# Optimization experiments

Measured on AMD Instinct MI355X. Metric: run time of the kernel, lower is better.

Reference implementation:

```python
import jax, jax.numpy as jnp
import numpy as np

B = 8192          # batch
DIM = 2048        # feature dim
FANOUT = 10       # balanced 10-ary tree, depth 3 -> 1000 leaves
N_NODES = 1 + 10 + 100  # inner nodes with classifiers = 111
NUM_CLASSES = 1000


def setup_inputs() -> dict:
    key = jax.random.key(0)
    k1, k2, k3, k4 = jax.random.split(key, 4)
    x = jax.random.normal(k1, (B, DIM), dtype=jnp.float32)
    labels = jax.random.randint(k2, (B,), 0, NUM_CLASSES, dtype=jnp.int64 if jax.config.jax_enable_x64 else jnp.int32)
    # Stacked per-node Linear(dim, num_child+1): column 0 is the extra slot
    # included in the softmax but never routed to (children use cols 1..FANOUT).
    W = jax.random.normal(k3, (N_NODES, DIM, FANOUT + 1), dtype=jnp.float32) * (1.0 / np.sqrt(DIM))
    b = jax.random.normal(k4, (N_NODES, FANOUT + 1), dtype=jnp.float32) * 0.01
    return {"x": x, "labels": labels, "W": W, "b": b}


def reference(x, labels, W, b):
    # All 111 tiny per-node Linear+softmax classifiers fused into one batched GEMM.
    logits = jnp.einsum('bd,ndk->bnk', x, W) + b          # [B, 111, 11]
    probs = jax.nn.softmax(logits, axis=-1)               # softmax over num_child+1 (incl. dummy col 0)
    # Hierarchical path probabilities (root.path_prob = 1.0):
    # level-1 nodes are children of root (node 0), via softmax columns 1..10.
    p1 = probs[:, 0, 1:]                                   # [B, 10]
    # level-2 nodes: children of nodes 1..10
    p2 = (p1[:, :, None] * probs[:, 1:11, 1:]).reshape(x.shape[0], 100)    # [B, 100]
    # leaves: children of nodes 11..110 -> 1000 classes (out[:, 1:] slice already applied)
    out = (p2[:, :, None] * probs[:, 11:111, 1:]).reshape(x.shape[0], NUM_CLASSES)  # [B, 1000]
    penalty = jnp.float32(0.0)
    return (out, penalty)
```

## Files before the change

kernel.cpp:

```cpp
#include <hip/hip_runtime.h>
#include <hip/hip_bf16.h>
#include <hip/hip_fp16.h>

typedef _Float16 f16;
typedef __attribute__((ext_vector_type(8))) _Float16 f16x8;
typedef __attribute__((ext_vector_type(4))) float f32x4;

#define DIM     2048
#define BROWS   8192
#define NCOLS   1221
#define NPAD    1280
#define NNODES  111
#define BM      128
#define BN      128
#define BK      64
#define NKT     (DIM / BK)
#define MT      (BROWS / BM)
#define NT      (NPAD / BN)

__global__ __launch_bounds__(256) void prep_x(const float* __restrict__ X,
                                              f16* __restrict__ Xf) {
    __shared__ float T[128 * 68];
    int blk = blockIdx.x;
    int mt = blk >> 5, kt = blk & 31;
    int t = threadIdx.x;
    int row = t >> 1, half = t & 1;
    const float* src = X + (size_t)(mt * 128 + row) * DIM + kt * 64 + half * 32;
    float* dst = T + row * 68 + half * 32;
    #pragma unroll
    for (int i = 0; i < 8; ++i) ((f32x4*)dst)[i] = ((const f32x4*)src)[i];
    __syncthreads();
    int w = t >> 6, l = t & 63, r = l & 15, q = l >> 4;
    f16* out = Xf + (size_t)blk * 8192;
    #pragma unroll
    for (int p = 0; p < 4; ++p) {
        int gk = p * 4 + w;
        int kk = gk >> 3, g = gk & 7;
        const float* s = T + (g * 16 + r) * 68 + kk * 32 + q * 8;
        f32x4 a = *(const f32x4*)s;
        f32x4 b = *(const f32x4*)(s + 4);
        f16x8 h;
        h[0] = (f16)a[0]; h[1] = (f16)a[1]; h[2] = (f16)a[2]; h[3] = (f16)a[3];
        h[4] = (f16)b[0]; h[5] = (f16)b[1]; h[6] = (f16)b[2]; h[7] = (f16)b[3];
        *(f16x8*)(out + (size_t)(p * 256 + t) * 8) = h;
    }
}

__global__ void prep_b(const float* __restrict__ W, f16* __restrict__ Bf) {
    int idx = blockIdx.x * 256 + threadIdx.x;
    int c = idx & 1023, img = idx >> 10;
    int nt = img >> 5, kt = img & 31;
    int kk = c >> 9, g = (c >> 6) & 7, l = c & 63, r = l & 15, q = l >> 4;
    int col = nt * 128 + g * 16 + r;
    int d0  = kt * 64 + kk * 32 + q * 8;
    f16x8 v;
    if (col < NCOLS) {
        int n = col / 11, k = col - n * 11;
        const float* src = W + ((size_t)n * DIM + d0) * 11 + k;
        #pragma unroll
        for (int e = 0; e < 8; ++e) v[e] = (f16)src[(size_t)e * 11];
    } else {
        #pragma unroll
        for (int e = 0; e < 8; ++e) v[e] = (f16)0.f;
    }
    *(f16x8*)(Bf + (size_t)idx * 8) = v;
}

__global__ __launch_bounds__(512) void gemm_f16(const f16* __restrict__ Xf,
                                                const f16* __restrict__ Bf,
                                                f16* __restrict__ Lh) {
    __shared__ __align__(16) f16 As[2][8192];
    __shared__ __align__(16) f16 Bs[2][8192];

    int bid = blockIdx.x;
    int swz = (bid & 7) * 80 + (bid >> 3);
    int mt = swz / 10, nt = swz - mt * 10;

    int t = threadIdx.x, w = t >> 6, l = t & 63, r = l & 15, q = l >> 4;
    int wm = w >> 2, wn = w & 3;

    const f16* abase = Xf + (size_t)(mt * 32) * 8192 + (size_t)t * 8;
    const f16* bbase = Bf + (size_t)(nt * 32) * 8192 + (size_t)t * 8;

    f32x4 acc[4][2];
    #pragma unroll
    for (int i = 0; i < 4; ++i)
        #pragma unroll
        for (int j = 0; j < 2; ++j) acc[i][j] = (f32x4)0.f;

#define STAGE(KT, C)                                                             \
    {                                                                            \
        const f16* asrc = abase + (size_t)(KT) * 8192;                           \
        const f16* bsrc = bbase + (size_t)(KT) * 8192;                           \
        _Pragma("unroll")                                                        \
        for (int p = 0; p < 2; ++p) {                                            \
            __builtin_amdgcn_global_load_lds(                                    \
                (const __attribute__((address_space(1))) void*)(asrc + p * 4096),\
                (__attribute__((address_space(3))) void*)(&As[C][p * 4096 + w * 512]), 16, 0, 0); \
            __builtin_amdgcn_global_load_lds(                                    \
                (const __attribute__((address_space(1))) void*)(bsrc + p * 4096),\
                (__attribute__((address_space(3))) void*)(&Bs[C][p * 4096 + w * 512]), 16, 0, 0); \
        }                                                                        \
    }

#define COMPUTE(C)                                                               \
    {                                                                            \
        _Pragma("unroll")                                                        \
        for (int kk = 0; kk < 2; ++kk) {                                         \
            f16x8 af[4], bfr[2];                                                 \
            _Pragma("unroll")                                                    \
            for (int m = 0; m < 4; ++m)                                          \
                af[m] = *(const f16x8*)(&As[C][((kk * 8 + wm * 4 + m) * 64 + l) * 8]); \
            _Pragma("unroll")                                                    \
            for (int n = 0; n < 2; ++n)                                          \
                bfr[n] = *(const f16x8*)(&Bs[C][((kk * 8 + wn * 2 + n) * 64 + l) * 8]); \
            _Pragma("unroll")                                                    \
            for (int m = 0; m < 4; ++m)                                          \
                _Pragma("unroll")                                                \
                for (int n = 0; n < 2; ++n)                                      \
                    acc[m][n] = __builtin_amdgcn_mfma_f32_16x16x32_f16(af[m], bfr[n], acc[m][n], 0, 0, 0); \
        }                                                                        \
    }

#define STEP(KTCUR, CC, CN)                                                      \
    {                                                                            \
        STAGE(KTCUR + 1, CN)                                                     \
        asm volatile("s_waitcnt vmcnt(4)" ::: "memory");                         \
        __builtin_amdgcn_s_barrier();                                            \
        COMPUTE(CC)                                                              \
        asm volatile("s_waitcnt lgkmcnt(0)" ::: "memory");                       \
        __builtin_amdgcn_s_barrier();                                            \
    }

    STAGE(0, 0)
    for (int kt = 0; kt < 30; kt += 2) {
        STEP(kt,     0, 1)
        STEP(kt + 1, 1, 0)
    }
    STEP(30, 0, 1)
    asm volatile("s_waitcnt vmcnt(0)" ::: "memory");
    __builtin_amdgcn_s_barrier();
    COMPUTE(1)

#undef STAGE
#undef COMPUTE
#undef STEP

    #pragma unroll
    for (int m = 0; m < 4; ++m) {
        int row = mt * 128 + wm * 64 + m * 16 + q * 4;
        #pragma unroll
        for (int n = 0; n < 2; ++n) {
            int col = nt * 128 + wn * 32 + n * 16 + r;
            #pragma unroll
            for (int j = 0; j < 4; ++j)
                Lh[(size_t)(row + j) * NPAD + col] = (f16)acc[m][n][j];
        }
    }
}

__global__ void tree_epi(const f16* __restrict__ L, const float* __restrict__ bias,
                         float* __restrict__ out) {
    __shared__ float P[4][NNODES * 11];
    __shared__ f16 R[4][NPAD];
    int w = threadIdx.x >> 6, l = threadIdx.x & 63;
    int row = blockIdx.x * 4 + w;

    const f16x8* src = (const f16x8*)(L + (size_t)row * NPAD);
    f16x8* dst = (f16x8*)R[w];
    dst[l]      = src[l];
    dst[l + 64] = src[l + 64];
    if (l < 32) dst[l + 128] = src[l + 128];

    for (int n = l; n < NNODES; n += 64) {
        float v[11], mx = -1e30f;
        #pragma unroll
        for (int k = 0; k < 11; ++k) { v[k] = (float)R[w][n * 11 + k] + bias[n * 11 + k]; mx = fmaxf(mx, v[k]); }
        float s = 0.f;
        #pragma unroll
        for (int k = 0; k < 11; ++k) { v[k] = __expf(v[k] - mx); s += v[k]; }
        float inv = 1.f / s;
        #pragma unroll
        for (int k = 0; k < 11; ++k) P[w][n * 11 + k] = v[k] * inv;
    }
    __syncthreads();
    const float* Pw = P[w];
    for (int c = l; c < 1000; c += 64) {
        int i  = c / 100;
        int j  = (c % 100) / 10;
        int mm = c % 10;
        float p = Pw[1 + i] * Pw[(1 + i) * 11 + 1 + j] * Pw[(11 + 10 * i + j) * 11 + 1 + mm];
        out[(size_t)row * 1000 + c] = p;
    }
    if (row == 0 && threadIdx.x == 0) out[(size_t)BROWS * 1000] = 0.f;
}

extern "C" void kernel_launch(void* const* d_in, const int* in_sizes, int n_in,
                              void* d_out, int out_size, void* d_ws, size_t ws_size,
                              hipStream_t stream) {
    const float* x    = (const float*)d_in[0];
    const float* W    = (const float*)d_in[2];
    const float* bias = (const float*)d_in[3];
    float* out = (float*)d_out;

    f16* Xf = (f16*)d_ws;
    f16* Bf = (f16*)((char*)d_ws + 33554432);
    f16* Lh = (f16*)((char*)d_ws + 38797312);

    prep_x <<<MT * 32, 256, 0, stream>>>(x, Xf);
    prep_b <<<1280, 256, 0, stream>>>(W, Bf);
    gemm_f16<<<MT * NT, 512, 0, stream>>>(Xf, Bf, Lh);
    tree_epi<<<BROWS / 4, 256, 0, stream>>>(Lh, bias, out);
}
```

Measured before the change: 93.30 us.

## Fuse fp32-to-fp16 conversion of X into the GEMM A-tile loader

Removes the separate prep_x kernel. The GEMM now loads fp32 X rows directly into registers, converts them to fp16, and writes them into a single XOR-swizzled LDS A buffer, while B keeps its double-buffered async global-to-LDS path. This drops one kernel launch and the round trip of writing and re-reading the fp16 copy of X. In exchange, every GEMM block reads A as fp32, which doubles A global and L2 traffic across the ten N-tiles, and the register-staged conversion adds latency to the pipeline.

Measured after the change: 108.6 us. +16.4%, slower.

```diff
diff --git a/kernel.cpp b/kernel.cpp
--- a/kernel.cpp
+++ b/kernel.cpp
@@ -18,34 +18,6 @@
 #define MT      (BROWS / BM)
 #define NT      (NPAD / BN)
 
-__global__ __launch_bounds__(256) void prep_x(const float* __restrict__ X,
-                                              f16* __restrict__ Xf) {
-    __shared__ float T[128 * 68];
-    int blk = blockIdx.x;
-    int mt = blk >> 5, kt = blk & 31;
-    int t = threadIdx.x;
-    int row = t >> 1, half = t & 1;
-    const float* src = X + (size_t)(mt * 128 + row) * DIM + kt * 64 + half * 32;
-    float* dst = T + row * 68 + half * 32;
-    #pragma unroll
-    for (int i = 0; i < 8; ++i) ((f32x4*)dst)[i] = ((const f32x4*)src)[i];
-    __syncthreads();
-    int w = t >> 6, l = t & 63, r = l & 15, q = l >> 4;
-    f16* out = Xf + (size_t)blk * 8192;
-    #pragma unroll
-    for (int p = 0; p < 4; ++p) {
-        int gk = p * 4 + w;
-        int kk = gk >> 3, g = gk & 7;
-        const float* s = T + (g * 16 + r) * 68 + kk * 32 + q * 8;
-        f32x4 a = *(const f32x4*)s;
-        f32x4 b = *(const f32x4*)(s + 4);
-        f16x8 h;
-        h[0] = (f16)a[0]; h[1] = (f16)a[1]; h[2] = (f16)a[2]; h[3] = (f16)a[3];
-        h[4] = (f16)b[0]; h[5] = (f16)b[1]; h[6] = (f16)b[2]; h[7] = (f16)b[3];
-        *(f16x8*)(out + (size_t)(p * 256 + t) * 8) = h;
-    }
-}
-
 __global__ void prep_b(const float* __restrict__ W, f16* __restrict__ Bf) {
     int idx = blockIdx.x * 256 + threadIdx.x;
     int c = idx & 1023, img = idx >> 10;
@@ -66,20 +38,27 @@
     *(f16x8*)(Bf + (size_t)idx * 8) = v;
 }
 
-__global__ __launch_bounds__(512) void gemm_f16(const f16* __restrict__ Xf,
+__global__ __launch_bounds__(512) void gemm_f16(const float* __restrict__ X,
                                                 const f16* __restrict__ Bf,
                                                 f16* __restrict__ Lh) {
-    __shared__ __align__(16) f16 As[2][8192];
+    __shared__ __align__(16) f16 As[8192];
     __shared__ __align__(16) f16 Bs[2][8192];
 
     int bid = blockIdx.x;
-    int swz = (bid & 7) * 80 + (bid >> 3);
-    int mt = swz / 10, nt = swz - mt * 10;
+    int swzb = (bid & 7) * 80 + (bid >> 3);
+    int mt = swzb / 10, nt = swzb - mt * 10;
 
     int t = threadIdx.x, w = t >> 6, l = t & 63, r = l & 15, q = l >> 4;
     int wm = w >> 2, wn = w & 3;
 
-    const f16* abase = Xf + (size_t)(mt * 32) * 8192 + (size_t)t * 8;
+    int arow = t >> 2, kc = t & 3;
+    const float* a_src = X + (size_t)(mt * 128 + arow) * DIM + kc * 16;
+    int kk_w = kc >> 1, g = arow >> 4, rr = arow & 15;
+    int q0 = (kc * 2) & 3, q1 = q0 + 1;
+    int wbyte0 = (((kk_w * 8 + g) * 1024) + q0 * 256 + rr * 16) ^ (q0 << 5) ^ (kk_w << 4);
+    int wbyte1 = (((kk_w * 8 + g) * 1024) + q1 * 256 + rr * 16) ^ (q1 << 5) ^ (kk_w << 4);
+    int ardo = (l * 16) ^ (q << 5);
+
     const f16* bbase = Bf + (size_t)(nt * 32) * 8192 + (size_t)t * 8;
 
     f32x4 acc[4][2];
@@ -88,32 +67,50 @@
         #pragma unroll
         for (int j = 0; j < 2; ++j) acc[i][j] = (f32x4)0.f;
 
-#define STAGE(KT, C)                                                             \
-    {                                                                            \
-        const f16* asrc = abase + (size_t)(KT) * 8192;                           \
+    f32x4 va0, va1, va2, va3;
+
+#define LOAD_A(KT)                                                               \
+    {                                                                            \
+        const float* s_ = a_src + (size_t)(KT) * BK;                             \
+        va0 = *(const f32x4*)(s_);      va1 = *(const f32x4*)(s_ + 4);           \
+        va2 = *(const f32x4*)(s_ + 8);  va3 = *(const f32x4*)(s_ + 12);          \
+    }
+
+#define CVT_WRITE_A()                                                            \
+    {                                                                            \
+        f16x8 h0, h1;                                                            \
+        _Pragma("unroll")                                                        \
+        for (int e = 0; e < 4; ++e) {                                            \
+            h0[e] = (f16)va0[e]; h0[e + 4] = (f16)va1[e];                        \
+            h1[e] = (f16)va2[e]; h1[e + 4] = (f16)va3[e];                        \
+        }                                                                        \
+        *(f16x8*)((char*)As + wbyte0) = h0;                                      \
+        *(f16x8*)((char*)As + wbyte1) = h1;                                      \
+    }
+
+#define STAGE_B(KT, CB)                                                          \
+    {                                                                            \
         const f16* bsrc = bbase + (size_t)(KT) * 8192;                           \
         _Pragma("unroll")                                                        \
         for (int p = 0; p < 2; ++p) {                                            \
             __builtin_amdgcn_global_load_lds(                                    \
-                (const __attribute__((address_space(1))) void*)(asrc + p * 4096),\
-                (__attribute__((address_space(3))) void*)(&As[C][p * 4096 + w * 512]), 16, 0, 0); \
-            __builtin_amdgcn_global_load_lds(                                    \
                 (const __attribute__((address_space(1))) void*)(bsrc + p * 4096),\
-                (__attribute__((address_space(3))) void*)(&Bs[C][p * 4096 + w * 512]), 16, 0, 0); \
+                (__attribute__((address_space(3))) void*)(&Bs[CB][p * 4096 + w * 512]), 16, 0, 0); \
         }                                                                        \
     }
 
-#define COMPUTE(C)                                                               \
+#define COMPUTE(CB)                                                              \
     {                                                                            \
         _Pragma("unroll")                                                        \
         for (int kk = 0; kk < 2; ++kk) {                                         \
             f16x8 af[4], bfr[2];                                                 \
             _Pragma("unroll")                                                    \
             for (int m = 0; m < 4; ++m)                                          \
-                af[m] = *(const f16x8*)(&As[C][((kk * 8 + wm * 4 + m) * 64 + l) * 8]); \
+                af[m] = *(const f16x8*)((char*)As + (kk * 8 + wm * 4 + m) * 1024 \
+                                        + (ardo ^ (kk << 4)));                   \
             _Pragma("unroll")                                                    \
             for (int n = 0; n < 2; ++n)                                          \
-                bfr[n] = *(const f16x8*)(&Bs[C][((kk * 8 + wn * 2 + n) * 64 + l) * 8]); \
+                bfr[n] = *(const f16x8*)(&Bs[CB][((kk * 8 + wn * 2 + n) * 64 + l) * 8]); \
             _Pragma("unroll")                                                    \
             for (int m = 0; m < 4; ++m)                                          \
                 _Pragma("unroll")                                                \
@@ -122,27 +119,34 @@
         }                                                                        \
     }
 
-#define STEP(KTCUR, CC, CN)                                                      \
-    {                                                                            \
-        STAGE(KTCUR + 1, CN)                                                     \
-        asm volatile("s_waitcnt vmcnt(4)" ::: "memory");                         \
+#define STEP(KT, CC, CN)                                                         \
+    {                                                                            \
+        CVT_WRITE_A()                                                            \
+        LOAD_A((KT) + 1)                                                         \
+        STAGE_B((KT) + 1, CN)                                                    \
+        asm volatile("s_waitcnt vmcnt(6) lgkmcnt(0)" ::: "memory");              \
         __builtin_amdgcn_s_barrier();                                            \
         COMPUTE(CC)                                                              \
         asm volatile("s_waitcnt lgkmcnt(0)" ::: "memory");                       \
         __builtin_amdgcn_s_barrier();                                            \
     }
 
-    STAGE(0, 0)
+    LOAD_A(0)
+    STAGE_B(0, 0)
+
     for (int kt = 0; kt < 30; kt += 2) {
         STEP(kt,     0, 1)
         STEP(kt + 1, 1, 0)
     }
     STEP(30, 0, 1)
-    asm volatile("s_waitcnt vmcnt(0)" ::: "memory");
+    CVT_WRITE_A()
+    asm volatile("s_waitcnt vmcnt(0) lgkmcnt(0)" ::: "memory");
     __builtin_amdgcn_s_barrier();
     COMPUTE(1)
 
-#undef STAGE
+#undef LOAD_A
+#undef CVT_WRITE_A
+#undef STAGE_B
 #undef COMPUTE
 #undef STEP
 
@@ -203,12 +207,10 @@
     const float* bias = (const float*)d_in[3];
     float* out = (float*)d_out;
 
-    f16* Xf = (f16*)d_ws;
-    f16* Bf = (f16*)((char*)d_ws + 33554432);
-    f16* Lh = (f16*)((char*)d_ws + 38797312);
-
-    prep_x <<<MT * 32, 256, 0, stream>>>(x, Xf);
+    f16* Bf = (f16*)d_ws;
+    f16* Lh = (f16*)((char*)d_ws + 5242880);
+
     prep_b <<<1280, 256, 0, stream>>>(W, Bf);
-    gemm_f16<<<MT * NT, 512, 0, stream>>>(Xf, Bf, Lh);
+    gemm_f16<<<MT * NT, 512, 0, stream>>>(x, Bf, Lh);
     tree_epi<<<BROWS / 4, 256, 0, stream>>>(Lh, bias, out);
 }
```
